# Kernel tuning notes

Hardware: AMD Instinct MI355X
Metric: run time of the kernel (lower is better)

## Reference

```python
import jax, jax.numpy as jnp
import numpy as np

N_NODES = 50000
N_EDGES = 800000


def setup_inputs() -> dict:
    key = jax.random.key(0)
    ks = jax.random.split(key, 8)
    x = jax.random.normal(ks[0], (N_NODES, 256), dtype=jnp.float32)
    edge_index = jax.random.randint(ks[1], (2, N_EDGES), 0, N_NODES, dtype=jnp.int64)
    edge_weight = jax.random.uniform(ks[2], (N_EDGES,), dtype=jnp.float32)
    # Glorot-style weights for the 3 GCNConv layers: 256->128->64->32
    def glorot(k, fan_in, fan_out):
        s = jnp.sqrt(6.0 / (fan_in + fan_out))
        return jax.random.uniform(k, (fan_in, fan_out), dtype=jnp.float32, minval=-s, maxval=s)
    return {
        "x": x,
        "edge_index": edge_index,
        "edge_weight": edge_weight,
        "W1": glorot(ks[3], 256, 128), "b1": jnp.zeros((128,), jnp.float32),
        "W2": glorot(ks[4], 128, 64),  "b2": jnp.zeros((64,), jnp.float32),
        "W3": glorot(ks[5], 64, 32),   "b3": jnp.zeros((32,), jnp.float32),
    }


def _gcn_forward(x, row, col, ew, params):
    """Stacked GCNConv+ReLU (PyG semantics: add self loops, symmetric norm)."""
    n = x.shape[0]
    loop = jnp.arange(n, dtype=row.dtype)
    row_f = jnp.concatenate([row, loop])            # [E+N] sources
    col_f = jnp.concatenate([col, loop])            # [E+N] targets
    ew_f = jnp.concatenate([ew, jnp.ones((n,), ew.dtype)])
    deg = jax.ops.segment_sum(ew_f, col_f, num_segments=n)
    dinv = jnp.where(deg > 0, jax.lax.rsqrt(deg), 0.0)
    norm = dinv[row_f] * ew_f * dinv[col_f]         # [E+N]
    for W, b in params:
        h = x @ W                                   # [N, d_out] linear first (PyG order)
        msg = h[row_f] * norm[:, None]              # [E+N, d_out] gather + scale
        agg = jax.ops.segment_sum(msg, col_f, num_segments=n)  # scatter-add
        x = jax.nn.relu(agg + b)                    # fused bias + ReLU
    return x


def reference(x, edge_index, edge_weight, W1, b1, W2, b2, W3, b3):
    row, col = edge_index[0], edge_index[1]
    params = [(W1, b1), (W2, b2), (W3, b3)]
    return _gcn_forward(x, row, col, edge_weight, params)
```

## Files before the change

kernel.cpp:

```cpp
#include <hip/hip_runtime.h>
#include <hip/hip_fp16.h>


#define D0 256
#define D1 128
#define D2 64
#define D3 32

#define FIX_SCALE 16777216.0f
#define FIX_INV   (1.0f / 16777216.0f)

typedef _Float16 half8 __attribute__((ext_vector_type(8)));
typedef float floatx4 __attribute__((ext_vector_type(4)));

__device__ __forceinline__ void stage_slab(const float* __restrict__ X, int slab,
                                           _Float16 (*__restrict__ sA)[D0 + 8], int t) {
    const int row = t >> 4;
    const int c0 = (t & 15) * 16;
    const float* src = X + (size_t)(slab * 16 + row) * D0 + c0;
    float4 f0 = *(const float4*)(src + 0);
    float4 f1 = *(const float4*)(src + 4);
    float4 f2 = *(const float4*)(src + 8);
    float4 f3 = *(const float4*)(src + 12);
    half8 h0, h1;
    h0[0] = (_Float16)f0.x; h0[1] = (_Float16)f0.y;
    h0[2] = (_Float16)f0.z; h0[3] = (_Float16)f0.w;
    h0[4] = (_Float16)f1.x; h0[5] = (_Float16)f1.y;
    h0[6] = (_Float16)f1.z; h0[7] = (_Float16)f1.w;
    h1[0] = (_Float16)f2.x; h1[1] = (_Float16)f2.y;
    h1[2] = (_Float16)f2.z; h1[3] = (_Float16)f2.w;
    h1[4] = (_Float16)f3.x; h1[5] = (_Float16)f3.y;
    h1[6] = (_Float16)f3.z; h1[7] = (_Float16)f3.w;
    *(half8*)&sA[row][c0]     = h0;
    *(half8*)&sA[row][c0 + 8] = h1;
}

__global__ __launch_bounds__(256) void hist_gemm1_kernel(
        const float* __restrict__ x, const float* __restrict__ W1,
        _Float16* __restrict__ h1, int N,
        const int* __restrict__ ei, const float* __restrict__ ew,
        unsigned long long* __restrict__ pk, int* __restrict__ rank, int E,
        int gB) {
    __shared__ _Float16 sA[2][16][D0 + 8];
    const int b = blockIdx.x;
    if (b >= gB) {
        int e = (b - gB) * 256 + threadIdx.x;
        if (e < E) {
            int c = ei[E + e];
            unsigned int wfix = (unsigned int)(ew[e] * FIX_SCALE + 0.5f);
            unsigned long long old =
                atomicAdd(&pk[c], (1ULL << 32) | (unsigned long long)wfix);
            rank[e] = (int)(old >> 32);
        }
        return;
    }
    constexpr int NC = D0 / 32;
    const int tid = threadIdx.x;
    const int w = tid >> 6;
    const int lane = tid & 63;
    const int quad = lane >> 4;
    const int m = lane & 15;
    const int n0 = w * 32;

    half8 b0[NC], b1[NC];
#pragma unroll
    for (int c = 0; c < NC; ++c) {
#pragma unroll
        for (int j = 0; j < 8; ++j) {
            int k = c * 32 + quad * 8 + j;
            b0[c][j] = (_Float16)W1[(size_t)k * D1 + n0 + m];
            b1[c][j] = (_Float16)W1[(size_t)k * D1 + n0 + 16 + m];
        }
    }

    const int nslab = N >> 4;
    int slab = b;
    if (slab >= nslab) return;
    stage_slab(x, slab, sA[0], tid);
    __syncthreads();
    int buf = 0;
    while (true) {
        const int next = slab + gB;
        if (next < nslab) stage_slab(x, next, sA[buf ^ 1], tid);

        half8 a[NC];
#pragma unroll
        for (int c = 0; c < NC; ++c)
            a[c] = *(const half8*)&sA[buf][m][c * 32 + quad * 8];
        floatx4 acc0 = (floatx4){0.f, 0.f, 0.f, 0.f};
        floatx4 acc1 = (floatx4){0.f, 0.f, 0.f, 0.f};
#pragma unroll
        for (int c = 0; c < NC; ++c) {
            acc0 = __builtin_amdgcn_mfma_f32_16x16x32_f16(a[c], b0[c], acc0, 0, 0, 0);
            acc1 = __builtin_amdgcn_mfma_f32_16x16x32_f16(a[c], b1[c], acc1, 0, 0, 0);
        }

        const int r0 = slab * 16 + quad * 4;
#pragma unroll
        for (int r = 0; r < 4; ++r) {
            h1[(size_t)(r0 + r) * D1 + n0 + m]      = (_Float16)acc0[r];
            h1[(size_t)(r0 + r) * D1 + n0 + 16 + m] = (_Float16)acc1[r];
        }
        __syncthreads();
        if (next >= nslab) break;
        slab = next;
        buf ^= 1;
    }
}

__global__ __launch_bounds__(256) void scan_reduce(const unsigned long long* __restrict__ pk,
                                                   float* __restrict__ dinv,
                                                   int* __restrict__ cnt,
                                                   int* __restrict__ blockSum, int N) {
    __shared__ int s[256];
    const int t = threadIdx.x;
    const int i = blockIdx.x * 256 + t;
    int v = 0;
    if (i < N) {
        unsigned long long p = pk[i];
        float d = (float)(unsigned int)(p & 0xffffffffULL) * FIX_INV + 1.0f;
        dinv[i] = rsqrtf(d);
        v = (int)(p >> 32);
        cnt[i] = v;
    }
    s[t] = v;
    __syncthreads();
#pragma unroll
    for (int off = 128; off > 0; off >>= 1) {
        if (t < off) s[t] += s[t + off];
        __syncthreads();
    }
    if (t == 0) blockSum[blockIdx.x] = s[0];
}

__global__ __launch_bounds__(256) void scan_apply(const int* __restrict__ cnt,
                                                  const int* __restrict__ blockSum,
                                                  int* __restrict__ row_ptr, int N, int B) {
    __shared__ int bs[256];
    __shared__ int s[256];
    const int t = threadIdx.x;
    bs[t] = (t < B) ? blockSum[t] : 0;
    __syncthreads();
#pragma unroll
    for (int off = 1; off < 256; off <<= 1) {
        int u = (t >= off) ? bs[t - off] : 0;
        __syncthreads();
        bs[t] += u;
        __syncthreads();
    }
    const int myOff = (blockIdx.x > 0) ? bs[blockIdx.x - 1] : 0;
    const int i = blockIdx.x * 256 + t;
    const int v = (i < N) ? cnt[i] : 0;
    s[t] = v;
    __syncthreads();
#pragma unroll
    for (int off = 1; off < 256; off <<= 1) {
        int u = (t >= off) ? s[t - off] : 0;
        __syncthreads();
        s[t] += u;
        __syncthreads();
    }
    if (i < N) row_ptr[i] = s[t] - v + myOff;
    if (blockIdx.x == 0 && t == 0) row_ptr[N] = bs[B - 1];
}

__global__ void fill_kernel(const int* __restrict__ ei, const float* __restrict__ ew,
                            const float* __restrict__ dinv,
                            const int* __restrict__ row_ptr, const int* __restrict__ rank,
                            int2* __restrict__ pairs, int E) {
    int e = blockIdx.x * blockDim.x + threadIdx.x;
    if (e < E) {
        int r = ei[e];
        int c = ei[E + e];
        float w = dinv[r] * ew[e] * dinv[c];
        pairs[row_ptr[c] + rank[e]] = make_int2(r, __float_as_int(w));
    }
}

template <int DIN, int DOUT>
__global__ __launch_bounds__(256) void agg_gemm_kernel(
        const _Float16* __restrict__ H, const int* __restrict__ row_ptr,
        const int2* __restrict__ pairs, const float* __restrict__ dinv,
        const float* __restrict__ bias, const float* __restrict__ W,
        _Float16* __restrict__ Hout, int N) {
    constexpr int TPN = DIN / 8;
    constexpr int NPB = 256 / TPN;
    constexpr int NC  = DIN / 32;
    constexpr int S   = NPB / 16;
    constexpr int T   = DOUT / 16;
    static_assert(S * T == 4, "one tile per wave");
    __shared__ _Float16 sA[NPB][DIN + 8];

    const int tid = threadIdx.x;
    const int g = tid / TPN;
    const int sl = tid % TPN;
    const int node0 = blockIdx.x * NPB;
    const int node = node0 + g;
    const bool valid = node < N;

    const int w = tid >> 6;
    const int lane = tid & 63;
    const int q = lane >> 4;
    const int m = lane & 15;
    const int s = w & (S - 1);
    const int t = w / S;
    half8 bf[NC];
#pragma unroll
    for (int c = 0; c < NC; ++c) {
#pragma unroll
        for (int j = 0; j < 8; ++j)
            bf[c][j] = (_Float16)W[(size_t)(c * 32 + q * 8 + j) * DOUT + t * 16 + m];
    }

    float acc[8];
#pragma unroll
    for (int j = 0; j < 8; ++j) acc[j] = 0.0f;

    int beg = 0, end = 0;
    float di = 0.f;
    half8 uself = (half8){0,0,0,0,0,0,0,0};
    float bb[8];
    if (valid) {
        beg = row_ptr[node];
        end = row_ptr[node + 1];
        di = dinv[node];
        uself = *(const half8*)&H[(size_t)node * DIN + sl * 8];
        *(float4*)&bb[0] = *(const float4*)&bias[sl * 8];
        *(float4*)&bb[4] = *(const float4*)&bias[sl * 8 + 4];
    }

    if (end > beg) {
        const int last = end - 1;
        int2 p0 = pairs[beg];
        int2 p1 = pairs[min(beg + 1, last)];
        int2 p2 = pairs[min(beg + 2, last)];
        int2 p3 = pairs[min(beg + 3, last)];
        int2 p4 = pairs[min(beg + 4, last)];
        half8 u0 = *(const half8*)&H[(size_t)p0.x * DIN + sl * 8];
        half8 u1 = *(const half8*)&H[(size_t)p1.x * DIN + sl * 8];
        half8 u2 = *(const half8*)&H[(size_t)p2.x * DIN + sl * 8];
        half8 u3 = *(const half8*)&H[(size_t)p3.x * DIN + sl * 8];
        for (int k = beg; k < end; ++k) {
            int2 p5 = pairs[min(k + 5, last)];
            half8 u4 = *(const half8*)&H[(size_t)p4.x * DIN + sl * 8];
            float wv = __int_as_float(p0.y);
#pragma unroll
            for (int j = 0; j < 8; ++j) acc[j] = fmaf(wv, (float)u0[j], acc[j]);
            p0 = p1; p1 = p2; p2 = p3; p3 = p4; p4 = p5;
            u0 = u1; u1 = u2; u2 = u3; u3 = u4;
        }
    }

    if (valid) {
        float d2 = di * di;
#pragma unroll
        for (int j = 0; j < 8; ++j) acc[j] = fmaf(d2, (float)uself[j], acc[j]);
        half8 o;
#pragma unroll
        for (int j = 0; j < 8; ++j) o[j] = (_Float16)fmaxf(acc[j] + bb[j], 0.f);
        *(half8*)&sA[g][sl * 8] = o;
    }
    __syncthreads();

    half8 a[NC];
#pragma unroll
    for (int c = 0; c < NC; ++c)
        a[c] = *(const half8*)&sA[s * 16 + m][c * 32 + q * 8];
    floatx4 o4 = (floatx4){0.f, 0.f, 0.f, 0.f};
#pragma unroll
    for (int c = 0; c < NC; ++c)
        o4 = __builtin_amdgcn_mfma_f32_16x16x32_f16(a[c], bf[c], o4, 0, 0, 0);
#pragma unroll
    for (int r = 0; r < 4; ++r) {
        const int nr = node0 + s * 16 + q * 4 + r;
        if (nr < N) Hout[(size_t)nr * DOUT + t * 16 + m] = (_Float16)o4[r];
    }
}

template <int D, typename OUT>
__global__ __launch_bounds__(256) void agg_kernel(const _Float16* __restrict__ H,
                                                  const int* __restrict__ row_ptr,
                                                  const int2* __restrict__ pairs,
                                                  const float* __restrict__ dinv,
                                                  const float* __restrict__ bias,
                                                  OUT* __restrict__ out, int N) {
    constexpr int TPN = D / 8;
    constexpr int NPB = 256 / TPN;
    const int tid = threadIdx.x;
    const int g = tid / TPN;
    const int lane = tid % TPN;
    const int node = blockIdx.x * NPB + g;
    if (node >= N) return;

    const int beg = row_ptr[node];
    const int end = row_ptr[node + 1];
    const float di = dinv[node];
    const half8 uself = *(const half8*)&H[(size_t)node * D + lane * 8];
    float b[8];
    *(float4*)&b[0] = *(const float4*)&bias[lane * 8];
    *(float4*)&b[4] = *(const float4*)&bias[lane * 8 + 4];

    float acc[8];
#pragma unroll
    for (int j = 0; j < 8; ++j) acc[j] = 0.0f;

    if (end > beg) {
        const int last = end - 1;
        int2 p0 = pairs[beg];
        int2 p1 = pairs[min(beg + 1, last)];
        int2 p2 = pairs[min(beg + 2, last)];
        int2 p3 = pairs[min(beg + 3, last)];
        int2 p4 = pairs[min(beg + 4, last)];
        half8 u0 = *(const half8*)&H[(size_t)p0.x * D + lane * 8];
        half8 u1 = *(const half8*)&H[(size_t)p1.x * D + lane * 8];
        half8 u2 = *(const half8*)&H[(size_t)p2.x * D + lane * 8];
        half8 u3 = *(const half8*)&H[(size_t)p3.x * D + lane * 8];
        for (int k = beg; k < end; ++k) {
            int2 p5 = pairs[min(k + 5, last)];
            half8 u4 = *(const half8*)&H[(size_t)p4.x * D + lane * 8];
            float w = __int_as_float(p0.y);
#pragma unroll
            for (int j = 0; j < 8; ++j) acc[j] = fmaf(w, (float)u0[j], acc[j]);
            p0 = p1; p1 = p2; p2 = p3; p3 = p4; p4 = p5;
            u0 = u1; u1 = u2; u2 = u3; u3 = u4;
        }
    }
    const float d2 = di * di;
#pragma unroll
    for (int j = 0; j < 8; ++j) acc[j] = fmaf(d2, (float)uself[j], acc[j]);
#pragma unroll
    for (int j = 0; j < 8; ++j) acc[j] = fmaxf(acc[j] + b[j], 0.f);

    if constexpr (sizeof(OUT) == 2) {
        half8 o;
#pragma unroll
        for (int j = 0; j < 8; ++j) o[j] = (_Float16)acc[j];
        *(half8*)&out[(size_t)node * D + lane * 8] = o;
    } else {
        float* dst = (float*)&out[(size_t)node * D + lane * 8];
        *(float4*)&dst[0] = make_float4(acc[0], acc[1], acc[2], acc[3]);
        *(float4*)&dst[4] = make_float4(acc[4], acc[5], acc[6], acc[7]);
    }
}

extern "C" void kernel_launch(void* const* d_in, const int* in_sizes, int n_in,
                              void* d_out, int out_size, void* d_ws, size_t ws_size,
                              hipStream_t stream) {
    const float* x   = (const float*)d_in[0];
    const int* ei    = (const int*)d_in[1];
    const float* ew  = (const float*)d_in[2];
    const float* W1  = (const float*)d_in[3];
    const float* b1  = (const float*)d_in[4];
    const float* W2  = (const float*)d_in[5];
    const float* b2  = (const float*)d_in[6];
    const float* W3  = (const float*)d_in[7];
    const float* b3  = (const float*)d_in[8];
    float* out = (float*)d_out;

    const int N = in_sizes[0] / D0;
    const int E = in_sizes[2];
    (void)n_in; (void)out_size; (void)ws_size;

    char* ws = (char*)d_ws;
    size_t off = 0;
    auto carve = [&](size_t bytes) -> void* {
        void* p = (void*)(ws + off);
        off += (bytes + 255) & ~(size_t)255;
        return p;
    };
    unsigned long long* pk = (unsigned long long*)carve((size_t)N * 8);
    float* dinv    = (float*)carve((size_t)N * 4);
    int*   cnt     = (int*)carve((size_t)N * 4);
    int*   row_ptr = (int*)carve((size_t)(N + 1) * 4);
    int*   rank    = (int*)carve((size_t)E * 4);
    int*   bsum    = (int*)carve(256 * 4);
    int2*  pairs   = (int2*)carve((size_t)E * 8);
    _Float16* bufH = (_Float16*)carve((size_t)N * D1 * 2);
    _Float16* bufO = (_Float16*)carve((size_t)N * D1 * 2);

    _Float16* h1 = bufH;
    _Float16* h2 = bufO;
    _Float16* h3 = bufH;

    const int eb = (E + 255) / 256;
    const int scanB = (N + 255) / 256;
    const int gB = 768;

    hipMemsetAsync(pk, 0, (size_t)N * 8, stream);
    hist_gemm1_kernel<<<gB + eb, 256, 0, stream>>>(
        x, W1, h1, N, ei, ew, pk, rank, E, gB);

    scan_reduce<<<scanB, 256, 0, stream>>>(pk, dinv, cnt, bsum, N);
    scan_apply<<<scanB, 256, 0, stream>>>(cnt, bsum, row_ptr, N, scanB);

    fill_kernel<<<eb, 256, 0, stream>>>(ei, ew, dinv, row_ptr, rank, pairs, E);

    agg_gemm_kernel<D1, D2><<<(N + 15) / 16, 256, 0, stream>>>(
        h1, row_ptr, pairs, dinv, b1, W2, h2, N);

    agg_gemm_kernel<D2, D3><<<(N + 31) / 32, 256, 0, stream>>>(
        h2, row_ptr, pairs, dinv, b2, W3, h3, N);

    agg_kernel<D3, float><<<(N + 63) / 64, 256, 0, stream>>>(
        h3, row_ptr, pairs, dinv, b3, out, N);
}
```

Baseline: 248.4 us.

## Fuse scan, fill and aggregation stages into one persistent kernel with grid barriers

Replaces six separate launches (scan reduce, scan apply, fill, two agg+GEMM layers, final aggregation) with a single persistent kernel of 768 blocks that walks each phase with grid-stride loops and uses an atomic-counter grid barrier between phases. The goal is to remove per-launch overhead and the idle tails between dependent kernels. In exchange it relies on all 768 blocks being co-resident (launch bounds of 4 blocks per CU), which risks deadlock if that does not hold. It also loses the parallelism of the original launch sizes and adds spin-wait cost at each barrier. The barrier state is zeroed by extending the existing memset.

```diff
diff --git a/kernel.cpp b/kernel.cpp
--- a/kernel.cpp
+++ b/kernel.cpp
@@ -9,9 +9,33 @@
 
 #define FIX_SCALE 16777216.0f
 #define FIX_INV   (1.0f / 16777216.0f)
+#define GRID 768
 
 typedef _Float16 half8 __attribute__((ext_vector_type(8)));
 typedef float floatx4 __attribute__((ext_vector_type(4)));
+
+struct GridBar { int cnt; int gen; };
+
+__device__ __forceinline__ void grid_sync(GridBar* bar, int nblk, int g) {
+    __syncthreads();
+    if (threadIdx.x == 0) {
+        __threadfence();
+        int arrived = __hip_atomic_fetch_add(&bar->cnt, 1, __ATOMIC_ACQ_REL,
+                                             __HIP_MEMORY_SCOPE_AGENT);
+        if (arrived == nblk - 1) {
+            __hip_atomic_store(&bar->cnt, 0, __ATOMIC_RELAXED,
+                               __HIP_MEMORY_SCOPE_AGENT);
+            __hip_atomic_store(&bar->gen, g + 1, __ATOMIC_RELEASE,
+                               __HIP_MEMORY_SCOPE_AGENT);
+        } else {
+            while (__hip_atomic_load(&bar->gen, __ATOMIC_ACQUIRE,
+                                     __HIP_MEMORY_SCOPE_AGENT) <= g) {
+                __builtin_amdgcn_s_sleep(2);
+            }
+        }
+    }
+    __syncthreads();
+}
 
 __device__ __forceinline__ void stage_slab(const float* __restrict__ X, int slab,
                                            _Float16 (*__restrict__ sA)[D0 + 8], int t) {
@@ -108,77 +132,8 @@
     }
 }
 
-__global__ __launch_bounds__(256) void scan_reduce(const unsigned long long* __restrict__ pk,
-                                                   float* __restrict__ dinv,
-                                                   int* __restrict__ cnt,
-                                                   int* __restrict__ blockSum, int N) {
-    __shared__ int s[256];
-    const int t = threadIdx.x;
-    const int i = blockIdx.x * 256 + t;
-    int v = 0;
-    if (i < N) {
-        unsigned long long p = pk[i];
-        float d = (float)(unsigned int)(p & 0xffffffffULL) * FIX_INV + 1.0f;
-        dinv[i] = rsqrtf(d);
-        v = (int)(p >> 32);
-        cnt[i] = v;
-    }
-    s[t] = v;
-    __syncthreads();
-#pragma unroll
-    for (int off = 128; off > 0; off >>= 1) {
-        if (t < off) s[t] += s[t + off];
-        __syncthreads();
-    }
-    if (t == 0) blockSum[blockIdx.x] = s[0];
-}
-
-__global__ __launch_bounds__(256) void scan_apply(const int* __restrict__ cnt,
-                                                  const int* __restrict__ blockSum,
-                                                  int* __restrict__ row_ptr, int N, int B) {
-    __shared__ int bs[256];
-    __shared__ int s[256];
-    const int t = threadIdx.x;
-    bs[t] = (t < B) ? blockSum[t] : 0;
-    __syncthreads();
-#pragma unroll
-    for (int off = 1; off < 256; off <<= 1) {
-        int u = (t >= off) ? bs[t - off] : 0;
-        __syncthreads();
-        bs[t] += u;
-        __syncthreads();
-    }
-    const int myOff = (blockIdx.x > 0) ? bs[blockIdx.x - 1] : 0;
-    const int i = blockIdx.x * 256 + t;
-    const int v = (i < N) ? cnt[i] : 0;
-    s[t] = v;
-    __syncthreads();
-#pragma unroll
-    for (int off = 1; off < 256; off <<= 1) {
-        int u = (t >= off) ? s[t - off] : 0;
-        __syncthreads();
-        s[t] += u;
-        __syncthreads();
-    }
-    if (i < N) row_ptr[i] = s[t] - v + myOff;
-    if (blockIdx.x == 0 && t == 0) row_ptr[N] = bs[B - 1];
-}
-
-__global__ void fill_kernel(const int* __restrict__ ei, const float* __restrict__ ew,
-                            const float* __restrict__ dinv,
-                            const int* __restrict__ row_ptr, const int* __restrict__ rank,
-                            int2* __restrict__ pairs, int E) {
-    int e = blockIdx.x * blockDim.x + threadIdx.x;
-    if (e < E) {
-        int r = ei[e];
-        int c = ei[E + e];
-        float w = dinv[r] * ew[e] * dinv[c];
-        pairs[row_ptr[c] + rank[e]] = make_int2(r, __float_as_int(w));
-    }
-}
-
 template <int DIN, int DOUT>
-__global__ __launch_bounds__(256) void agg_gemm_kernel(
+__device__ void agg_gemm_phase(char* smemRaw,
         const _Float16* __restrict__ H, const int* __restrict__ row_ptr,
         const int2* __restrict__ pairs, const float* __restrict__ dinv,
         const float* __restrict__ bias, const float* __restrict__ W,
@@ -189,21 +144,18 @@
     constexpr int S   = NPB / 16;
     constexpr int T   = DOUT / 16;
     static_assert(S * T == 4, "one tile per wave");
-    __shared__ _Float16 sA[NPB][DIN + 8];
+    _Float16 (*sA)[DIN + 8] = (_Float16 (*)[DIN + 8])smemRaw;
 
     const int tid = threadIdx.x;
-    const int g = tid / TPN;
+    const int grp = tid / TPN;
     const int sl = tid % TPN;
-    const int node0 = blockIdx.x * NPB;
-    const int node = node0 + g;
-    const bool valid = node < N;
-
     const int w = tid >> 6;
     const int lane = tid & 63;
     const int q = lane >> 4;
     const int m = lane & 15;
     const int s = w & (S - 1);
     const int t = w / S;
+
     half8 bf[NC];
 #pragma unroll
     for (int c = 0; c < NC; ++c) {
@@ -212,135 +164,228 @@
             bf[c][j] = (_Float16)W[(size_t)(c * 32 + q * 8 + j) * DOUT + t * 16 + m];
     }
 
-    float acc[8];
-#pragma unroll
-    for (int j = 0; j < 8; ++j) acc[j] = 0.0f;
-
-    int beg = 0, end = 0;
-    float di = 0.f;
-    half8 uself = (half8){0,0,0,0,0,0,0,0};
-    float bb[8];
-    if (valid) {
-        beg = row_ptr[node];
-        end = row_ptr[node + 1];
-        di = dinv[node];
-        uself = *(const half8*)&H[(size_t)node * DIN + sl * 8];
-        *(float4*)&bb[0] = *(const float4*)&bias[sl * 8];
-        *(float4*)&bb[4] = *(const float4*)&bias[sl * 8 + 4];
-    }
-
-    if (end > beg) {
-        const int last = end - 1;
-        int2 p0 = pairs[beg];
-        int2 p1 = pairs[min(beg + 1, last)];
-        int2 p2 = pairs[min(beg + 2, last)];
-        int2 p3 = pairs[min(beg + 3, last)];
-        int2 p4 = pairs[min(beg + 4, last)];
-        half8 u0 = *(const half8*)&H[(size_t)p0.x * DIN + sl * 8];
-        half8 u1 = *(const half8*)&H[(size_t)p1.x * DIN + sl * 8];
-        half8 u2 = *(const half8*)&H[(size_t)p2.x * DIN + sl * 8];
-        half8 u3 = *(const half8*)&H[(size_t)p3.x * DIN + sl * 8];
-        for (int k = beg; k < end; ++k) {
-            int2 p5 = pairs[min(k + 5, last)];
-            half8 u4 = *(const half8*)&H[(size_t)p4.x * DIN + sl * 8];
-            float wv = __int_as_float(p0.y);
-#pragma unroll
-            for (int j = 0; j < 8; ++j) acc[j] = fmaf(wv, (float)u0[j], acc[j]);
-            p0 = p1; p1 = p2; p2 = p3; p3 = p4; p4 = p5;
-            u0 = u1; u1 = u2; u2 = u3; u3 = u4;
-        }
-    }
-
-    if (valid) {
-        float d2 = di * di;
-#pragma unroll
-        for (int j = 0; j < 8; ++j) acc[j] = fmaf(d2, (float)uself[j], acc[j]);
-        half8 o;
-#pragma unroll
-        for (int j = 0; j < 8; ++j) o[j] = (_Float16)fmaxf(acc[j] + bb[j], 0.f);
-        *(half8*)&sA[g][sl * 8] = o;
-    }
-    __syncthreads();
-
-    half8 a[NC];
-#pragma unroll
-    for (int c = 0; c < NC; ++c)
-        a[c] = *(const half8*)&sA[s * 16 + m][c * 32 + q * 8];
-    floatx4 o4 = (floatx4){0.f, 0.f, 0.f, 0.f};
-#pragma unroll
-    for (int c = 0; c < NC; ++c)
-        o4 = __builtin_amdgcn_mfma_f32_16x16x32_f16(a[c], bf[c], o4, 0, 0, 0);
-#pragma unroll
-    for (int r = 0; r < 4; ++r) {
-        const int nr = node0 + s * 16 + q * 4 + r;
-        if (nr < N) Hout[(size_t)nr * DOUT + t * 16 + m] = (_Float16)o4[r];
-    }
-}
-
-template <int D, typename OUT>
-__global__ __launch_bounds__(256) void agg_kernel(const _Float16* __restrict__ H,
-                                                  const int* __restrict__ row_ptr,
-                                                  const int2* __restrict__ pairs,
-                                                  const float* __restrict__ dinv,
-                                                  const float* __restrict__ bias,
-                                                  OUT* __restrict__ out, int N) {
+    const int nvb = (N + NPB - 1) / NPB;
+    for (int vb = blockIdx.x; vb < nvb; vb += gridDim.x) {
+        const int node0 = vb * NPB;
+        const int node = node0 + grp;
+        const bool valid = node < N;
+
+        float acc[8];
+#pragma unroll
+        for (int j = 0; j < 8; ++j) acc[j] = 0.0f;
+
+        int beg = 0, end = 0;
+        float di = 0.f;
+        half8 uself = (half8){0,0,0,0,0,0,0,0};
+        float bb[8];
+        if (valid) {
+            beg = row_ptr[node];
+            end = row_ptr[node + 1];
+            di = dinv[node];
+            uself = *(const half8*)&H[(size_t)node * DIN + sl * 8];
+            *(float4*)&bb[0] = *(const float4*)&bias[sl * 8];
+            *(float4*)&bb[4] = *(const float4*)&bias[sl * 8 + 4];
+        }
+
+        if (end > beg) {
+            const int last = end - 1;
+            int2 p0 = pairs[beg];
+            int2 p1 = pairs[min(beg + 1, last)];
+            int2 p2 = pairs[min(beg + 2, last)];
+            int2 p3 = pairs[min(beg + 3, last)];
+            int2 p4 = pairs[min(beg + 4, last)];
+            half8 u0 = *(const half8*)&H[(size_t)p0.x * DIN + sl * 8];
+            half8 u1 = *(const half8*)&H[(size_t)p1.x * DIN + sl * 8];
+            half8 u2 = *(const half8*)&H[(size_t)p2.x * DIN + sl * 8];
+            half8 u3 = *(const half8*)&H[(size_t)p3.x * DIN + sl * 8];
+            for (int k = beg; k < end; ++k) {
+                int2 p5 = pairs[min(k + 5, last)];
+                half8 u4 = *(const half8*)&H[(size_t)p4.x * DIN + sl * 8];
+                float wv = __int_as_float(p0.y);
+#pragma unroll
+                for (int j = 0; j < 8; ++j) acc[j] = fmaf(wv, (float)u0[j], acc[j]);
+                p0 = p1; p1 = p2; p2 = p3; p3 = p4; p4 = p5;
+                u0 = u1; u1 = u2; u2 = u3; u3 = u4;
+            }
+        }
+
+        if (valid) {
+            float d2 = di * di;
+#pragma unroll
+            for (int j = 0; j < 8; ++j) acc[j] = fmaf(d2, (float)uself[j], acc[j]);
+            half8 o;
+#pragma unroll
+            for (int j = 0; j < 8; ++j) o[j] = (_Float16)fmaxf(acc[j] + bb[j], 0.f);
+            *(half8*)&sA[grp][sl * 8] = o;
+        }
+        __syncthreads();
+
+        half8 a[NC];
+#pragma unroll
+        for (int c = 0; c < NC; ++c)
+            a[c] = *(const half8*)&sA[s * 16 + m][c * 32 + q * 8];
+        floatx4 o4 = (floatx4){0.f, 0.f, 0.f, 0.f};
+#pragma unroll
+        for (int c = 0; c < NC; ++c)
+            o4 = __builtin_amdgcn_mfma_f32_16x16x32_f16(a[c], bf[c], o4, 0, 0, 0);
+#pragma unroll
+        for (int r = 0; r < 4; ++r) {
+            const int nr = node0 + s * 16 + q * 4 + r;
+            if (nr < N) Hout[(size_t)nr * DOUT + t * 16 + m] = (_Float16)o4[r];
+        }
+        __syncthreads();
+    }
+}
+
+__device__ void agg_final_phase(const _Float16* __restrict__ H,
+        const int* __restrict__ row_ptr, const int2* __restrict__ pairs,
+        const float* __restrict__ dinv, const float* __restrict__ bias,
+        float* __restrict__ out, int N) {
+    constexpr int D = D3;
     constexpr int TPN = D / 8;
     constexpr int NPB = 256 / TPN;
     const int tid = threadIdx.x;
-    const int g = tid / TPN;
+    const int grp = tid / TPN;
     const int lane = tid % TPN;
-    const int node = blockIdx.x * NPB + g;
-    if (node >= N) return;
-
-    const int beg = row_ptr[node];
-    const int end = row_ptr[node + 1];
-    const float di = dinv[node];
-    const half8 uself = *(const half8*)&H[(size_t)node * D + lane * 8];
-    float b[8];
-    *(float4*)&b[0] = *(const float4*)&bias[lane * 8];
-    *(float4*)&b[4] = *(const float4*)&bias[lane * 8 + 4];
-
-    float acc[8];
-#pragma unroll
-    for (int j = 0; j < 8; ++j) acc[j] = 0.0f;
-
-    if (end > beg) {
-        const int last = end - 1;
-        int2 p0 = pairs[beg];
-        int2 p1 = pairs[min(beg + 1, last)];
-        int2 p2 = pairs[min(beg + 2, last)];
-        int2 p3 = pairs[min(beg + 3, last)];
-        int2 p4 = pairs[min(beg + 4, last)];
-        half8 u0 = *(const half8*)&H[(size_t)p0.x * D + lane * 8];
-        half8 u1 = *(const half8*)&H[(size_t)p1.x * D + lane * 8];
-        half8 u2 = *(const half8*)&H[(size_t)p2.x * D + lane * 8];
-        half8 u3 = *(const half8*)&H[(size_t)p3.x * D + lane * 8];
-        for (int k = beg; k < end; ++k) {
-            int2 p5 = pairs[min(k + 5, last)];
-            half8 u4 = *(const half8*)&H[(size_t)p4.x * D + lane * 8];
-            float w = __int_as_float(p0.y);
-#pragma unroll
-            for (int j = 0; j < 8; ++j) acc[j] = fmaf(w, (float)u0[j], acc[j]);
-            p0 = p1; p1 = p2; p2 = p3; p3 = p4; p4 = p5;
-            u0 = u1; u1 = u2; u2 = u3; u3 = u4;
-        }
-    }
-    const float d2 = di * di;
-#pragma unroll
-    for (int j = 0; j < 8; ++j) acc[j] = fmaf(d2, (float)uself[j], acc[j]);
-#pragma unroll
-    for (int j = 0; j < 8; ++j) acc[j] = fmaxf(acc[j] + b[j], 0.f);
-
-    if constexpr (sizeof(OUT) == 2) {
-        half8 o;
-#pragma unroll
-        for (int j = 0; j < 8; ++j) o[j] = (_Float16)acc[j];
-        *(half8*)&out[(size_t)node * D + lane * 8] = o;
-    } else {
-        float* dst = (float*)&out[(size_t)node * D + lane * 8];
+    const int nvb = (N + NPB - 1) / NPB;
+    for (int vb = blockIdx.x; vb < nvb; vb += gridDim.x) {
+        const int node = vb * NPB + grp;
+        if (node >= N) continue;
+
+        const int beg = row_ptr[node];
+        const int end = row_ptr[node + 1];
+        const float di = dinv[node];
+        const half8 uself = *(const half8*)&H[(size_t)node * D + lane * 8];
+        float b[8];
+        *(float4*)&b[0] = *(const float4*)&bias[lane * 8];
+        *(float4*)&b[4] = *(const float4*)&bias[lane * 8 + 4];
+
+        float acc[8];
+#pragma unroll
+        for (int j = 0; j < 8; ++j) acc[j] = 0.0f;
+
+        if (end > beg) {
+            const int last = end - 1;
+            int2 p0 = pairs[beg];
+            int2 p1 = pairs[min(beg + 1, last)];
+            int2 p2 = pairs[min(beg + 2, last)];
+            int2 p3 = pairs[min(beg + 3, last)];
+            int2 p4 = pairs[min(beg + 4, last)];
+            half8 u0 = *(const half8*)&H[(size_t)p0.x * D + lane * 8];
+            half8 u1 = *(const half8*)&H[(size_t)p1.x * D + lane * 8];
+            half8 u2 = *(const half8*)&H[(size_t)p2.x * D + lane * 8];
+            half8 u3 = *(const half8*)&H[(size_t)p3.x * D + lane * 8];
+            for (int k = beg; k < end; ++k) {
+                int2 p5 = pairs[min(k + 5, last)];
+                half8 u4 = *(const half8*)&H[(size_t)p4.x * D + lane * 8];
+                float w = __int_as_float(p0.y);
+#pragma unroll
+                for (int j = 0; j < 8; ++j) acc[j] = fmaf(w, (float)u0[j], acc[j]);
+                p0 = p1; p1 = p2; p2 = p3; p3 = p4; p4 = p5;
+                u0 = u1; u1 = u2; u2 = u3; u3 = u4;
+            }
+        }
+        const float d2 = di * di;
+#pragma unroll
+        for (int j = 0; j < 8; ++j) acc[j] = fmaf(d2, (float)uself[j], acc[j]);
+#pragma unroll
+        for (int j = 0; j < 8; ++j) acc[j] = fmaxf(acc[j] + b[j], 0.f);
+
+        float* dst = &out[(size_t)node * D + lane * 8];
         *(float4*)&dst[0] = make_float4(acc[0], acc[1], acc[2], acc[3]);
         *(float4*)&dst[4] = make_float4(acc[4], acc[5], acc[6], acc[7]);
     }
+}
+
+__global__ __launch_bounds__(256, 4) void mega_kernel(
+        const unsigned long long* __restrict__ pk,
+        float* __restrict__ dinv, int* __restrict__ cnt,
+        int* __restrict__ row_ptr, int* __restrict__ bsum,
+        const int* __restrict__ ei, const float* __restrict__ ew,
+        const int* __restrict__ rank, int2* __restrict__ pairs,
+        const _Float16* __restrict__ h1,
+        const float* __restrict__ b1, const float* __restrict__ W2,
+        _Float16* __restrict__ h2,
+        const float* __restrict__ b2, const float* __restrict__ W3,
+        _Float16* __restrict__ h3,
+        const float* __restrict__ b3, float* __restrict__ out,
+        GridBar* bar, int N, int E, int scanB) {
+    __shared__ __align__(16) char smem[4608];
+    const int t = threadIdx.x;
+    const int nblk = gridDim.x;
+
+    {
+        int* s = (int*)smem;
+        for (int vb = blockIdx.x; vb < scanB; vb += nblk) {
+            const int i = vb * 256 + t;
+            int v = 0;
+            if (i < N) {
+                unsigned long long p = pk[i];
+                float d = (float)(unsigned int)(p & 0xffffffffULL) * FIX_INV + 1.0f;
+                dinv[i] = rsqrtf(d);
+                v = (int)(p >> 32);
+                cnt[i] = v;
+            }
+            s[t] = v;
+            __syncthreads();
+#pragma unroll
+            for (int off = 128; off > 0; off >>= 1) {
+                if (t < off) s[t] += s[t + off];
+                __syncthreads();
+            }
+            if (t == 0) bsum[vb] = s[0];
+            __syncthreads();
+        }
+    }
+    grid_sync(bar, nblk, 0);
+
+    {
+        int* bs = (int*)smem;
+        int* s = (int*)smem + 256;
+        for (int vb = blockIdx.x; vb < scanB; vb += nblk) {
+            bs[t] = (t < scanB) ? bsum[t] : 0;
+            __syncthreads();
+#pragma unroll
+            for (int off = 1; off < 256; off <<= 1) {
+                int u = (t >= off) ? bs[t - off] : 0;
+                __syncthreads();
+                bs[t] += u;
+                __syncthreads();
+            }
+            const int myOff = (vb > 0) ? bs[vb - 1] : 0;
+            const int i = vb * 256 + t;
+            const int v = (i < N) ? cnt[i] : 0;
+            s[t] = v;
+            __syncthreads();
+#pragma unroll
+            for (int off = 1; off < 256; off <<= 1) {
+                int u = (t >= off) ? s[t - off] : 0;
+                __syncthreads();
+                s[t] += u;
+                __syncthreads();
+            }
+            if (i < N) row_ptr[i] = s[t] - v + myOff;
+            if (vb == 0 && t == 0) row_ptr[N] = bs[scanB - 1];
+            __syncthreads();
+        }
+    }
+    grid_sync(bar, nblk, 1);
+
+    for (int e = blockIdx.x * 256 + t; e < E; e += nblk * 256) {
+        int r = ei[e];
+        int c = ei[E + e];
+        float w = dinv[r] * ew[e] * dinv[c];
+        pairs[row_ptr[c] + rank[e]] = make_int2(r, __float_as_int(w));
+    }
+    grid_sync(bar, nblk, 2);
+
+    agg_gemm_phase<D1, D2>(smem, h1, row_ptr, pairs, dinv, b1, W2, h2, N);
+    grid_sync(bar, nblk, 3);
+
+    agg_gemm_phase<D2, D3>(smem, h2, row_ptr, pairs, dinv, b2, W3, h3, N);
+    grid_sync(bar, nblk, 4);
+
+    agg_final_phase(h3, row_ptr, pairs, dinv, b3, out, N);
 }
 
 extern "C" void kernel_launch(void* const* d_in, const int* in_sizes, int n_in,
@@ -368,7 +413,9 @@
         off += (bytes + 255) & ~(size_t)255;
         return p;
     };
+    const size_t pkBytes = ((size_t)N * 8 + 255) & ~(size_t)255;
     unsigned long long* pk = (unsigned long long*)carve((size_t)N * 8);
+    GridBar* bar   = (GridBar*)carve(256);
     float* dinv    = (float*)carve((size_t)N * 4);
     int*   cnt     = (int*)carve((size_t)N * 4);
     int*   row_ptr = (int*)carve((size_t)(N + 1) * 4);
@@ -386,21 +433,13 @@
     const int scanB = (N + 255) / 256;
     const int gB = 768;
 
-    hipMemsetAsync(pk, 0, (size_t)N * 8, stream);
+    hipMemsetAsync(pk, 0, pkBytes + 256, stream);
+
     hist_gemm1_kernel<<<gB + eb, 256, 0, stream>>>(
         x, W1, h1, N, ei, ew, pk, rank, E, gB);
 
-    scan_reduce<<<scanB, 256, 0, stream>>>(pk, dinv, cnt, bsum, N);
-    scan_apply<<<scanB, 256, 0, stream>>>(cnt, bsum, row_ptr, N, scanB);
-
-    fill_kernel<<<eb, 256, 0, stream>>>(ei, ew, dinv, row_ptr, rank, pairs, E);
-
-    agg_gemm_kernel<D1, D2><<<(N + 15) / 16, 256, 0, stream>>>(
-        h1, row_ptr, pairs, dinv, b1, W2, h2, N);
-
-    agg_gemm_kernel<D2, D3><<<(N + 31) / 32, 256, 0, stream>>>(
-        h2, row_ptr, pairs, dinv, b2, W3, h3, N);
-
-    agg_kernel<D3, float><<<(N + 63) / 64, 256, 0, stream>>>(
-        h3, row_ptr, pairs, dinv, b3, out, N);
-}
+    mega_kernel<<<GRID, 256, 0, stream>>>(
+        pk, dinv, cnt, row_ptr, bsum, ei, ew, rank, pairs,
+        h1, b1, W2, h2, b2, W3, h3, b3, out,
+        bar, N, E, scanB);
+}
```

Measured after the change: 946.2 us. 3.81x slower.

## Split each node's edge list across multiple thread groups in layers 2 and 3

Applied to the files above, without the earlier changes.

Replaces the layer-2 and layer-3 aggregation kernels with versions that assign several thread sub-groups per node, each walking a strided subset of the node's edges. Partial sums are then combined through shared memory before the self-loop, bias, ReLU and (for layer 2) the MFMA projection. The aim is more memory-level parallelism and shorter per-thread dependency chains on the narrow feature widths, where each node previously had only a few threads. The cost is extra shared-memory reductions, block-wide syncs, and idle threads in the reduce and GEMM phases.

```diff
diff --git a/kernel.cpp b/kernel.cpp
--- a/kernel.cpp
+++ b/kernel.cpp
@@ -277,47 +277,133 @@
     }
 }
 
-template <int D, typename OUT>
-__global__ __launch_bounds__(256) void agg_kernel(const _Float16* __restrict__ H,
-                                                  const int* __restrict__ row_ptr,
-                                                  const int2* __restrict__ pairs,
-                                                  const float* __restrict__ dinv,
-                                                  const float* __restrict__ bias,
-                                                  OUT* __restrict__ out, int N) {
-    constexpr int TPN = D / 8;
-    constexpr int NPB = 256 / TPN;
+__global__ __launch_bounds__(256) void agg2_split_kernel(
+        const _Float16* __restrict__ H, const int* __restrict__ row_ptr,
+        const int2* __restrict__ pairs, const float* __restrict__ dinv,
+        const float* __restrict__ bias, const float* __restrict__ W,
+        _Float16* __restrict__ Hout, int N) {
+    __shared__ float pacc[16][64];
+    __shared__ _Float16 sA[16][D2 + 8];
     const int tid = threadIdx.x;
-    const int g = tid / TPN;
-    const int lane = tid % TPN;
-    const int node = blockIdx.x * NPB + g;
-    if (node >= N) return;
-
-    const int beg = row_ptr[node];
-    const int end = row_ptr[node + 1];
-    const float di = dinv[node];
-    const half8 uself = *(const half8*)&H[(size_t)node * D + lane * 8];
-    float b[8];
-    *(float4*)&b[0] = *(const float4*)&bias[lane * 8];
-    *(float4*)&b[4] = *(const float4*)&bias[lane * 8 + 4];
+    const int grp = tid >> 4;
+    const int sub = (tid >> 3) & 1;
+    const int sl  = tid & 7;
+    const int node0 = blockIdx.x * 16;
+    const int node = node0 + grp;
+    const bool valid = node < N;
 
     float acc[8];
 #pragma unroll
     for (int j = 0; j < 8; ++j) acc[j] = 0.0f;
 
-    if (end > beg) {
+    int beg = 0, end = 0;
+    if (valid) { beg = row_ptr[node]; end = row_ptr[node + 1]; }
+
+    const int kb = beg + sub;
+    if (end > kb) {
         const int last = end - 1;
-        int2 p0 = pairs[beg];
-        int2 p1 = pairs[min(beg + 1, last)];
-        int2 p2 = pairs[min(beg + 2, last)];
-        int2 p3 = pairs[min(beg + 3, last)];
-        int2 p4 = pairs[min(beg + 4, last)];
-        half8 u0 = *(const half8*)&H[(size_t)p0.x * D + lane * 8];
-        half8 u1 = *(const half8*)&H[(size_t)p1.x * D + lane * 8];
-        half8 u2 = *(const half8*)&H[(size_t)p2.x * D + lane * 8];
-        half8 u3 = *(const half8*)&H[(size_t)p3.x * D + lane * 8];
-        for (int k = beg; k < end; ++k) {
-            int2 p5 = pairs[min(k + 5, last)];
-            half8 u4 = *(const half8*)&H[(size_t)p4.x * D + lane * 8];
+        int2 p0 = pairs[min(kb,     last)];
+        int2 p1 = pairs[min(kb + 2, last)];
+        int2 p2 = pairs[min(kb + 4, last)];
+        int2 p3 = pairs[min(kb + 6, last)];
+        int2 p4 = pairs[min(kb + 8, last)];
+        half8 u0 = *(const half8*)&H[(size_t)p0.x * D2 + sl * 8];
+        half8 u1 = *(const half8*)&H[(size_t)p1.x * D2 + sl * 8];
+        half8 u2 = *(const half8*)&H[(size_t)p2.x * D2 + sl * 8];
+        half8 u3 = *(const half8*)&H[(size_t)p3.x * D2 + sl * 8];
+        for (int k = kb; k < end; k += 2) {
+            int2 p5 = pairs[min(k + 10, last)];
+            half8 u4 = *(const half8*)&H[(size_t)p4.x * D2 + sl * 8];
+            float wv = __int_as_float(p0.y);
+#pragma unroll
+            for (int j = 0; j < 8; ++j) acc[j] = fmaf(wv, (float)u0[j], acc[j]);
+            p0 = p1; p1 = p2; p2 = p3; p3 = p4; p4 = p5;
+            u0 = u1; u1 = u2; u2 = u3; u3 = u4;
+        }
+    }
+    if (valid && sub == 1) {
+        *(float4*)&pacc[grp][sl * 8]     = make_float4(acc[0], acc[1], acc[2], acc[3]);
+        *(float4*)&pacc[grp][sl * 8 + 4] = make_float4(acc[4], acc[5], acc[6], acc[7]);
+    }
+    __syncthreads();
+    if (valid && sub == 0) {
+        const float4 q0 = *(const float4*)&pacc[grp][sl * 8];
+        const float4 q1 = *(const float4*)&pacc[grp][sl * 8 + 4];
+        acc[0] += q0.x; acc[1] += q0.y; acc[2] += q0.z; acc[3] += q0.w;
+        acc[4] += q1.x; acc[5] += q1.y; acc[6] += q1.z; acc[7] += q1.w;
+        const float di = dinv[node];
+        const float d2 = di * di;
+        const half8 uself = *(const half8*)&H[(size_t)node * D2 + sl * 8];
+#pragma unroll
+        for (int j = 0; j < 8; ++j) acc[j] = fmaf(d2, (float)uself[j], acc[j]);
+        float bb[8];
+        *(float4*)&bb[0] = *(const float4*)&bias[sl * 8];
+        *(float4*)&bb[4] = *(const float4*)&bias[sl * 8 + 4];
+        half8 o;
+#pragma unroll
+        for (int j = 0; j < 8; ++j) o[j] = (_Float16)fmaxf(acc[j] + bb[j], 0.f);
+        *(half8*)&sA[grp][sl * 8] = o;
+    }
+    __syncthreads();
+
+    const int w = tid >> 6;
+    const int lane = tid & 63;
+    const int q = lane >> 4;
+    const int m = lane & 15;
+    if (w < 2) {
+        half8 bf[2], a[2];
+#pragma unroll
+        for (int c = 0; c < 2; ++c) {
+#pragma unroll
+            for (int j = 0; j < 8; ++j)
+                bf[c][j] = (_Float16)W[(size_t)(c * 32 + q * 8 + j) * D3 + w * 16 + m];
+            a[c] = *(const half8*)&sA[m][c * 32 + q * 8];
+        }
+        floatx4 o4 = (floatx4){0.f, 0.f, 0.f, 0.f};
+        o4 = __builtin_amdgcn_mfma_f32_16x16x32_f16(a[0], bf[0], o4, 0, 0, 0);
+        o4 = __builtin_amdgcn_mfma_f32_16x16x32_f16(a[1], bf[1], o4, 0, 0, 0);
+#pragma unroll
+        for (int r = 0; r < 4; ++r) {
+            const int nr = node0 + q * 4 + r;
+            if (nr < N) Hout[(size_t)nr * D3 + w * 16 + m] = (_Float16)o4[r];
+        }
+    }
+}
+
+__global__ __launch_bounds__(256) void agg3_split_kernel(
+        const _Float16* __restrict__ H, const int* __restrict__ row_ptr,
+        const int2* __restrict__ pairs, const float* __restrict__ dinv,
+        const float* __restrict__ bias, float* __restrict__ out, int N) {
+    __shared__ float pacc[16][3][32];
+    const int tid = threadIdx.x;
+    const int grp = tid >> 4;
+    const int sub = (tid >> 2) & 3;
+    const int sl  = tid & 3;
+    const int node = blockIdx.x * 16 + grp;
+    const bool valid = node < N;
+
+    float acc[8];
+#pragma unroll
+    for (int j = 0; j < 8; ++j) acc[j] = 0.0f;
+
+    int beg = 0, end = 0;
+    if (valid) { beg = row_ptr[node]; end = row_ptr[node + 1]; }
+
+    const int kb = beg + sub;
+    if (end > kb) {
+        const int last = end - 1;
+        int2 p0 = pairs[min(kb,      last)];
+        int2 p1 = pairs[min(kb + 4,  last)];
+        int2 p2 = pairs[min(kb + 8,  last)];
+        int2 p3 = pairs[min(kb + 12, last)];
+        int2 p4 = pairs[min(kb + 16, last)];
+        half8 u0 = *(const half8*)&H[(size_t)p0.x * D3 + sl * 8];
+        half8 u1 = *(const half8*)&H[(size_t)p1.x * D3 + sl * 8];
+        half8 u2 = *(const half8*)&H[(size_t)p2.x * D3 + sl * 8];
+        half8 u3 = *(const half8*)&H[(size_t)p3.x * D3 + sl * 8];
+        for (int k = kb; k < end; k += 4) {
+            int2 p5 = pairs[min(k + 20, last)];
+            half8 u4 = *(const half8*)&H[(size_t)p4.x * D3 + sl * 8];
             float w = __int_as_float(p0.y);
 #pragma unroll
             for (int j = 0; j < 8; ++j) acc[j] = fmaf(w, (float)u0[j], acc[j]);
@@ -325,19 +411,30 @@
             u0 = u1; u1 = u2; u2 = u3; u3 = u4;
         }
     }
-    const float d2 = di * di;
-#pragma unroll
-    for (int j = 0; j < 8; ++j) acc[j] = fmaf(d2, (float)uself[j], acc[j]);
-#pragma unroll
-    for (int j = 0; j < 8; ++j) acc[j] = fmaxf(acc[j] + b[j], 0.f);
-
-    if constexpr (sizeof(OUT) == 2) {
-        half8 o;
-#pragma unroll
-        for (int j = 0; j < 8; ++j) o[j] = (_Float16)acc[j];
-        *(half8*)&out[(size_t)node * D + lane * 8] = o;
-    } else {
-        float* dst = (float*)&out[(size_t)node * D + lane * 8];
+    if (valid && sub > 0) {
+        *(float4*)&pacc[grp][sub - 1][sl * 8]     = make_float4(acc[0], acc[1], acc[2], acc[3]);
+        *(float4*)&pacc[grp][sub - 1][sl * 8 + 4] = make_float4(acc[4], acc[5], acc[6], acc[7]);
+    }
+    __syncthreads();
+    if (valid && sub == 0) {
+#pragma unroll
+        for (int s = 0; s < 3; ++s) {
+            const float4 q0 = *(const float4*)&pacc[grp][s][sl * 8];
+            const float4 q1 = *(const float4*)&pacc[grp][s][sl * 8 + 4];
+            acc[0] += q0.x; acc[1] += q0.y; acc[2] += q0.z; acc[3] += q0.w;
+            acc[4] += q1.x; acc[5] += q1.y; acc[6] += q1.z; acc[7] += q1.w;
+        }
+        const float di = dinv[node];
+        const float d2 = di * di;
+        const half8 uself = *(const half8*)&H[(size_t)node * D3 + sl * 8];
+#pragma unroll
+        for (int j = 0; j < 8; ++j) acc[j] = fmaf(d2, (float)uself[j], acc[j]);
+        float bb[8];
+        *(float4*)&bb[0] = *(const float4*)&bias[sl * 8];
+        *(float4*)&bb[4] = *(const float4*)&bias[sl * 8 + 4];
+#pragma unroll
+        for (int j = 0; j < 8; ++j) acc[j] = fmaxf(acc[j] + bb[j], 0.f);
+        float* dst = &out[(size_t)node * D3 + sl * 8];
         *(float4*)&dst[0] = make_float4(acc[0], acc[1], acc[2], acc[3]);
         *(float4*)&dst[4] = make_float4(acc[4], acc[5], acc[6], acc[7]);
     }
@@ -398,9 +495,9 @@
     agg_gemm_kernel<D1, D2><<<(N + 15) / 16, 256, 0, stream>>>(
         h1, row_ptr, pairs, dinv, b1, W2, h2, N);
 
-    agg_gemm_kernel<D2, D3><<<(N + 31) / 32, 256, 0, stream>>>(
+    agg2_split_kernel<<<(N + 15) / 16, 256, 0, stream>>>(
         h2, row_ptr, pairs, dinv, b2, W3, h3, N);
 
-    agg_kernel<D3, float><<<(N + 63) / 64, 256, 0, stream>>>(
+    agg3_split_kernel<<<(N + 15) / 16, 256, 0, stream>>>(
         h3, row_ptr, pairs, dinv, b3, out, N);
 }
```

Measured after the change: 243.0 us (median of 2 runs). 2.2% less time.
